# Kernel optimization log

Hardware: AMD Instinct MI355X
Metric: run time of the kernel (lower is better)

The kernel has to match this reference:

```python
import jax, jax.numpy as jnp
import numpy as np

B, SL = 16, 512
S = SL - 1            # context length after shift (length=1)
E = 256               # embedding_size / hidden_size
NH = 4                # num_heads
K = 4                 # conv1d_kernel_size
I = 2 * E             # mLSTM inner dim (_inner_embedding_dim = 2*E)
DHM = I // NH         # mLSTM head dim
DHS = E // NH         # sLSTM head dim
NB, BS = I // 4, 4    # qkv_proj_blocksize=4 block-diagonal projections
F = 384               # gated FFN up dim = round_up(1.3*256, 64)
NUM_SKILLS, NUM_Q = 500, 10000
EPS = 1e-5


def _ln(x, w):
    mu = x.mean(-1, keepdims=True)
    var = x.var(-1, keepdims=True)
    return (x - mu) / jnp.sqrt(var + EPS) * w


def _causal_dwconv(x, w, b):
    # x: (B,S,C), depthwise causal conv with kernel (C,K)
    xt = jnp.transpose(x, (0, 2, 1))
    y = jax.lax.conv_general_dilated(
        xt, w[:, None, :], (1,), [(K - 1, 0)],
        dimension_numbers=('NCH', 'OIH', 'NCH'),
        feature_group_count=x.shape[-1])
    return jnp.transpose(y, (0, 2, 1)) + b


def _headwise(x, w):
    # block-diagonal linear: w (NB, BS, BS)
    xb = x.reshape(x.shape[0], x.shape[1], NB, BS)
    return jnp.einsum('bsnd,nod->bsno', xb, w).reshape(x.shape)


def _forward(questions, responses, skills,
             q_embed, qa_embed, q_embed_diff, qa_embed_diff, difficult_param,
             ln0_w, m_up_w, m_up_b, m_conv_w, m_conv_b, m_q_w, m_k_w, m_v_w,
             m_ig_w, m_ig_b, m_fg_w, m_fg_b, m_outnorm_w, m_skip, m_down_w, m_down_b,
             ln1_w, s_conv_w, s_conv_b, s_gate_w, s_rec_w, s_bias, s_gn_w,
             ln2_w, ffn_up_w, ffn_up_b, ffn_down_w, ffn_down_b,
             postnorm_w, out_w1, out_b1, out_w2, out_b2, out_w3, out_b3):
    pid = questions[:, :-1]
    q_data = skills[:, :-1]
    q_shft = skills[:, 1:]
    target = (responses * (responses > -1).astype(responses.dtype))[:, :-1]

    q_e = q_embed[q_data]                              # (B,S,E)
    qa_e = qa_embed[target] + q_e
    pid_e = difficult_param[pid]                       # (B,S,1)
    q_e = q_e + pid_e * q_embed_diff[q_data]
    qa_e = qa_e + pid_e * qa_embed_diff[target]

    # ---- xLSTM stack: block 0 = mLSTM block, block 1 = sLSTM block + gated FFN ----
    x = qa_e  # dropout is identity in eval

    # mLSTM block: x = x + mlstm_layer(LN(x))
    h = _ln(x, ln0_w)
    up = h @ m_up_w.T + m_up_b                         # (B,S,2I)
    x_m, z = jnp.split(up, 2, axis=-1)
    xc = jax.nn.silu(_causal_dwconv(x_m, m_conv_w, m_conv_b))
    q = _headwise(xc, m_q_w)
    k = _headwise(xc, m_k_w)
    v = _headwise(x_m, m_v_w)
    ifin = jnp.concatenate([q, k, v], axis=-1)         # (B,S,3I)
    ig = jnp.einsum('bsf,hf->bhs', ifin, m_ig_w) + m_ig_b[None, :, None]
    fg = jnp.einsum('bsf,hf->bhs', ifin, m_fg_w) + m_fg_b[None, :, None]
    qh = q.reshape(B, S, NH, DHM).transpose(0, 2, 1, 3)
    kh = k.reshape(B, S, NH, DHM).transpose(0, 2, 1, 3)
    vh = v.reshape(B, S, NH, DHM).transpose(0, 2, 1, 3)
    # parallel stabilized mLSTM
    logf = jax.nn.log_sigmoid(fg)                      # (B,NH,S)
    cs = jnp.concatenate([jnp.zeros((B, NH, 1), logf.dtype), jnp.cumsum(logf, -1)], -1)
    dmat = cs[:, :, 1:, None] - cs[:, :, None, 1:]     # (B,NH,S,S): sum of logf over (s,t]
    ltr = jnp.tril(jnp.ones((S, S), bool))
    logD = jnp.where(ltr, dmat, -jnp.inf) + ig[:, :, None, :]
    maxD = jnp.max(logD, -1, keepdims=True)
    D = jnp.exp(logD - maxD)
    qk = jnp.einsum('bhtd,bhsd->bhts', qh, kh) * (DHM ** -0.5)
    C = qk * D
    norm = jnp.maximum(jnp.abs(C.sum(-1, keepdims=True)), jnp.exp(-maxD))
    hh = jnp.einsum('bhts,bhsd->bhtd', C / (norm + 1e-6), vh)
    # multi-head layernorm (per head over DHM), weight on flattened dim
    hn = (hh - hh.mean(-1, keepdims=True)) / jnp.sqrt(hh.var(-1, keepdims=True) + EPS)
    hflat = hn.transpose(0, 2, 1, 3).reshape(B, S, I) * m_outnorm_w
    hout = (hflat + m_skip * xc) * jax.nn.silu(z)
    x = x + (hout @ m_down_w.T + m_down_b)

    # sLSTM block: x = x + slstm_layer(LN(x)); x = x + ffn(LN(x))
    h = _ln(x, ln1_w)
    hc = jax.nn.silu(_causal_dwconv(h, s_conv_w, s_conv_b))
    hh4 = h.reshape(B, S, NH, DHS)
    hc4 = hc.reshape(B, S, NH, DHS)
    gi = jnp.einsum('bsnd,nod->bsno', hc4, s_gate_w[0])   # i,f from conv path
    gf = jnp.einsum('bsnd,nod->bsno', hc4, s_gate_w[1])
    gz = jnp.einsum('bsnd,nod->bsno', hh4, s_gate_w[2])   # z,o from x path
    go = jnp.einsum('bsnd,nod->bsno', hh4, s_gate_w[3])
    wx = jnp.stack([gi, gf, gz, go], axis=2) + s_bias[None, None]  # (B,S,4,NH,DHS)

    def step(carry, wx_t):
        y, c, n, m = carry
        raw = wx_t + jnp.einsum('bnd,gnde->bgne', y, s_rec_w)
        iraw, fraw, zraw, oraw = raw[:, 0], raw[:, 1], raw[:, 2], raw[:, 3]
        logfplusm = m + jax.nn.log_sigmoid(fraw)
        mnew = jnp.maximum(iraw, logfplusm)
        ig_ = jnp.exp(iraw - mnew)
        fg_ = jnp.exp(logfplusm - mnew)
        cnew = fg_ * c + ig_ * jnp.tanh(zraw)
        nnew = fg_ * n + ig_
        ynew = jax.nn.sigmoid(oraw) * cnew / nnew
        return (ynew, cnew, nnew, mnew), ynew

    z0 = jnp.zeros((B, NH, DHS), x.dtype)
    _, ys = jax.lax.scan(step, (z0, z0, z0, z0), jnp.swapaxes(wx, 0, 1))
    y = jnp.swapaxes(ys, 0, 1)                           # (B,S,NH,DHS)
    yn = (y - y.mean(-1, keepdims=True)) / jnp.sqrt(y.var(-1, keepdims=True) + EPS)
    x = x + yn.reshape(B, S, E) * s_gn_w

    # gated FFN (relu)
    h = _ln(x, ln2_w)
    gate, upf = jnp.split(h @ ffn_up_w.T + ffn_up_b, 2, axis=-1)
    x = x + (jax.nn.relu(gate) * upf) @ ffn_down_w.T + ffn_down_b

    d = _ln(x, postnorm_w)                               # post_blocks_norm

    fam = jnp.where((target == 1)[..., None], d, 0.0)
    unfam = jnp.where((target == 0)[..., None], d, 0.0)
    d2 = d - pid_e
    cq = jnp.concatenate([d2, q_e, fam, unfam], axis=-1)  # (B,S,4E)
    o = jax.nn.relu(cq @ out_w1.T + out_b1)
    o = jax.nn.relu(o @ out_w2.T + out_b2)
    probs = jax.nn.sigmoid(o @ out_w3.T + out_b3)
    pred = jnp.take_along_axis(probs, q_shft[..., None], axis=-1)[..., 0]
    return pred                                          # (B,S)


def setup_inputs():
    key = jax.random.key(0)
    ks = iter(jax.random.split(key, 64))
    def rn(shape, s=0.02):
        return jax.random.normal(next(ks), shape, jnp.float32) * s
    return dict(
        questions=jax.random.randint(next(ks), (B, SL), 0, NUM_Q),
        responses=jax.random.randint(next(ks), (B, SL), 0, 2),
        skills=jax.random.randint(next(ks), (B, SL), 0, NUM_SKILLS),
        attention_mask=jnp.ones((B, SL), jnp.int32),
        q_embed=rn((NUM_SKILLS, E), 1.0),
        qa_embed=rn((2, E), 1.0),
        q_embed_diff=rn((NUM_SKILLS + 1, E), 1.0),
        qa_embed_diff=rn((2 * NUM_SKILLS + 1, E), 1.0),
        difficult_param=rn((NUM_Q + 1, 1), 0.1),
        ln0_w=jnp.ones((E,)),
        m_up_w=rn((2 * I, E)), m_up_b=jnp.zeros((2 * I,)),
        m_conv_w=rn((I, K), 0.1), m_conv_b=jnp.zeros((I,)),
        m_q_w=rn((NB, BS, BS), 0.1), m_k_w=rn((NB, BS, BS), 0.1), m_v_w=rn((NB, BS, BS), 0.1),
        m_ig_w=rn((NH, 3 * I)), m_ig_b=jnp.zeros((NH,)),
        m_fg_w=rn((NH, 3 * I)), m_fg_b=jnp.zeros((NH,)),
        m_outnorm_w=jnp.ones((I,)), m_skip=jnp.ones((I,)),
        m_down_w=rn((E, I)), m_down_b=jnp.zeros((E,)),
        ln1_w=jnp.ones((E,)),
        s_conv_w=rn((E, K), 0.1), s_conv_b=jnp.zeros((E,)),
        s_gate_w=rn((4, NH, DHS, DHS), 0.1),
        s_rec_w=rn((4, NH, DHS, DHS), 0.05),
        s_bias=jnp.zeros((4, NH, DHS)),
        s_gn_w=jnp.ones((E,)),
        ln2_w=jnp.ones((E,)),
        ffn_up_w=rn((2 * F, E)), ffn_up_b=jnp.zeros((2 * F,)),
        ffn_down_w=rn((E, F)), ffn_down_b=jnp.zeros((E,)),
        postnorm_w=jnp.ones((E,)),
        out_w1=rn((2 * E, 4 * E)), out_b1=jnp.zeros((2 * E,)),
        out_w2=rn((E, 2 * E)), out_b2=jnp.zeros((E,)),
        out_w3=rn((NUM_SKILLS, E)), out_b3=jnp.zeros((NUM_SKILLS,)),
    )


def reference(questions, responses, skills, attention_mask,
              q_embed, qa_embed, q_embed_diff, qa_embed_diff, difficult_param,
              ln0_w, m_up_w, m_up_b, m_conv_w, m_conv_b, m_q_w, m_k_w, m_v_w,
              m_ig_w, m_ig_b, m_fg_w, m_fg_b, m_outnorm_w, m_skip, m_down_w, m_down_b,
              ln1_w, s_conv_w, s_conv_b, s_gate_w, s_rec_w, s_bias, s_gn_w,
              ln2_w, ffn_up_w, ffn_up_b, ffn_down_w, ffn_down_b,
              postnorm_w, out_w1, out_b1, out_w2, out_b2, out_w3, out_b3):
    return _forward(questions, responses, skills,
                    q_embed, qa_embed, q_embed_diff, qa_embed_diff, difficult_param,
                    ln0_w, m_up_w, m_up_b, m_conv_w, m_conv_b, m_q_w, m_k_w, m_v_w,
                    m_ig_w, m_ig_b, m_fg_w, m_fg_b, m_outnorm_w, m_skip, m_down_w, m_down_b,
                    ln1_w, s_conv_w, s_conv_b, s_gate_w, s_rec_w, s_bias, s_gn_w,
                    ln2_w, ffn_up_w, ffn_up_b, ffn_down_w, ffn_down_b,
                    postnorm_w, out_w1, out_b1, out_w2, out_b2, out_w3, out_b3)
```

## Files before the change

kernel.cpp:

```cpp
#include <hip/hip_runtime.h>
#include <hip/hip_bf16.h>

#define B_    16
#define SL_   512
#define S_    511
#define E_    256
#define NH_   4
#define I_    512
#define DHM_  128
#define DHS_  64
#define F_    384
#define NP_   8192
#define NROW  (B_*S_)
#define EPS_  1e-5f

typedef __hip_bfloat16 bf16;
typedef unsigned short u16;
typedef __bf16 bf16x8v __attribute__((ext_vector_type(8)));
typedef float  f32x4v  __attribute__((ext_vector_type(4)));

__device__ __forceinline__ float rcp_(float x){ return __builtin_amdgcn_rcpf(x); }
__device__ __forceinline__ float sig_(float x){ return rcp_(1.f+__expf(-x)); }
__device__ __forceinline__ float silu_(float x){ return x*sig_(x); }
__device__ __forceinline__ float logsig_(float x){ return fminf(x,0.f) - __logf(1.f + __expf(-fabsf(x))); }
__device__ __forceinline__ float expneg_(float x){ return __expf(fminf(x,0.f)); }
__device__ __forceinline__ float expclamp_(float x){ return __expf(fminf(fmaxf(x,-80.f),80.f)); }
__device__ __forceinline__ float tanh_(float x){ return 1.f - 2.f*rcp_(__expf(2.f*x)+1.f); }

__device__ __forceinline__ void cvt_split8(const float* __restrict__ p, bf16x8v& hv, bf16x8v& lv){
  float4 u = *(const float4*)p;
  float4 w = *(const float4*)(p+4);
  float x[8] = {u.x,u.y,u.z,u.w,w.x,w.y,w.z,w.w};
  union { bf16x8v v; u16 s[8]; } H, L;
  #pragma unroll
  for(int j=0;j<8;j++){
    bf16 hh = __float2bfloat16(x[j]);
    float hf = __bfloat162float(hh);
    bf16 ll = __float2bfloat16(x[j]-hf);
    __builtin_memcpy(&H.s[j],&hh,2);
    __builtin_memcpy(&L.s[j],&ll,2);
  }
  hv=H.v; lv=L.v;
}

__global__ __launch_bounds__(256) void k_cvt16(const float* __restrict__ src, bf16* __restrict__ dst, int n){
  int i=blockIdx.x*256+threadIdx.x;
  if(i<n) dst[i]=__float2bfloat16(src[i]);
}
__global__ __launch_bounds__(256) void k_cvt16i(const float* __restrict__ src, bf16* __restrict__ dst){
  int i=blockIdx.x*256+threadIdx.x;
  int rp=i>>8, c=i&255;
  int j=rp>>1, p=rp&1;
  dst[i]=__float2bfloat16(src[(size_t)(j + p*F_)*E_ + c]);
}
__global__ __launch_bounds__(256) void k_cvtsplit(const float* __restrict__ src,
  bf16* __restrict__ hi, bf16* __restrict__ lo, int n){
  int i=blockIdx.x*256+threadIdx.x;
  if(i<n){
    float v=src[i];
    bf16 h=__float2bfloat16(v);
    hi[i]=h;
    lo[i]=__float2bfloat16(v-__bfloat162float(h));
  }
}
__global__ __launch_bounds__(256) void k_wtrans(const float* __restrict__ src, float* __restrict__ dst){
  int i = blockIdx.x*256+threadIdx.x;
  int blk = i>>12;
  int d = (i>>6)&63;
  int e = i&63;
  dst[(size_t)(blk*64+d)*64+e] = src[(size_t)(blk*64+e)*64+d];
}

__global__ __launch_bounds__(256) void k_wfrag(const float* __restrict__ rw, bf16* __restrict__ wf){
  int i = blockIdx.x*256+threadIdx.x;
  int j  = i&7;
  int l  = (i>>3)&63;
  int kf = (i>>9)&1;
  int t  = (i>>10)&15;
  int n  = i>>14;
  int g = t>>2;
  int e = (t&3)*16 + (l&15);
  int d = (l>>4)*16 + kf*8 + j;
  wf[i] = __float2bfloat16(rw[((size_t)((g*4+n)*64 + d))*64 + e]);
}

__global__ __launch_bounds__(256) void k_embed(
  const int* __restrict__ questions, const int* __restrict__ responses, const int* __restrict__ skills,
  const float* __restrict__ q_embed, const float* __restrict__ qa_embed,
  const float* __restrict__ q_embed_diff, const float* __restrict__ qa_embed_diff,
  const float* __restrict__ difficult_param, const float* __restrict__ ln0w,
  float* __restrict__ x, float* __restrict__ qe,
  bf16* __restrict__ h_hi, bf16* __restrict__ h_lo,
  float* __restrict__ pide, int* __restrict__ tgt, int* __restrict__ qsh)
{
  __shared__ float red[256];
  int r = blockIdx.x; int e = threadIdx.x;
  float xa = 0.f;
  if (r < NROW){
    int b = r / S_, s = r % S_;
    int pid  = questions[b*SL_+s];
    int qd   = skills[b*SL_+s];
    int resp = responses[b*SL_+s];
    int t    = (resp > -1) ? resp : 0;
    float pe = difficult_param[pid];
    float q0 = q_embed[qd*E_+e];
    xa = q0 + qa_embed[t*E_+e] + pe*qa_embed_diff[t*E_+e];
    float qn = q0 + pe*q_embed_diff[qd*E_+e];
    x[(size_t)r*E_+e]=xa; qe[(size_t)r*E_+e]=qn;
    if (e==0){ pide[r]=pe; tgt[r]=t; qsh[r]=skills[b*SL_+s+1]; }
  } else {
    x[(size_t)r*E_+e]=0.f; qe[(size_t)r*E_+e]=0.f;
    if (e==0){ pide[r]=0.f; tgt[r]=-7; qsh[r]=0; }
  }
  red[e]=xa; __syncthreads();
  for(int s2=128;s2>0;s2>>=1){ if(e<s2) red[e]+=red[e+s2]; __syncthreads(); }
  float mu = red[0]*(1.f/E_); __syncthreads();
  float d = xa-mu;
  red[e]=d*d; __syncthreads();
  for(int s2=128;s2>0;s2>>=1){ if(e<s2) red[e]+=red[e+s2]; __syncthreads(); }
  float var = red[0]*(1.f/E_);
  float o = d*rsqrtf(var+EPS_)*ln0w[e];
  bf16 hv = __float2bfloat16(o);
  h_hi[(size_t)r*E_+e] = hv;
  h_lo[(size_t)r*E_+e] = __float2bfloat16(o-__bfloat162float(hv));
}

__global__ __launch_bounds__(256) void k_ln(
  const float* __restrict__ in, const float* __restrict__ w, float* __restrict__ out)
{
  __shared__ float red[256];
  int r = blockIdx.x, t = threadIdx.x;
  float v = in[(size_t)r*E_+t];
  red[t]=v; __syncthreads();
  for(int s=128;s>0;s>>=1){ if(t<s) red[t]+=red[t+s]; __syncthreads(); }
  float mu = red[0]*(1.f/E_); __syncthreads();
  float d = v-mu;
  red[t]=d*d; __syncthreads();
  for(int s=128;s>0;s>>=1){ if(t<s) red[t]+=red[t+s]; __syncthreads(); }
  float var = red[0]*(1.f/E_);
  out[(size_t)r*E_+t] = d*rsqrtf(var+EPS_)*w[t];
}

__global__ __launch_bounds__(256) void k_gemm16s(
  const bf16* __restrict__ Ah, const bf16* __restrict__ Al,
  const bf16* __restrict__ Bh, const bf16* __restrict__ Bl,
  const float* __restrict__ bias, float* __restrict__ C, int M, int K)
{
  int tid=threadIdx.x;
  int wave=tid>>6, lane=tid&63;
  int wr=wave>>1, wc=wave&1;
  int row0=blockIdx.y*64 + wr*32;
  int col0=blockIdx.x*64 + wc*32;
  int lrow = lane&15, lq = lane>>4;
  f32x4v acc[2][2] = {};
  size_t aoff = (size_t)(row0+lrow)*K + lq*8;
  size_t boff = (size_t)(col0+lrow)*K + lq*8;
  for(int k0=0;k0<K;k0+=32){
    bf16x8v ah0=*(const bf16x8v*)(Ah+aoff+k0), ah1=*(const bf16x8v*)(Ah+aoff+(size_t)16*K+k0);
    bf16x8v al0=*(const bf16x8v*)(Al+aoff+k0), al1=*(const bf16x8v*)(Al+aoff+(size_t)16*K+k0);
    bf16x8v bh0=*(const bf16x8v*)(Bh+boff+k0), bh1=*(const bf16x8v*)(Bh+boff+(size_t)16*K+k0);
    bf16x8v bl0=*(const bf16x8v*)(Bl+boff+k0), bl1=*(const bf16x8v*)(Bl+boff+(size_t)16*K+k0);
    acc[0][0]=__builtin_amdgcn_mfma_f32_16x16x32_bf16(ah0,bh0,acc[0][0],0,0,0);
    acc[0][1]=__builtin_amdgcn_mfma_f32_16x16x32_bf16(ah0,bh1,acc[0][1],0,0,0);
    acc[1][0]=__builtin_amdgcn_mfma_f32_16x16x32_bf16(ah1,bh0,acc[1][0],0,0,0);
    acc[1][1]=__builtin_amdgcn_mfma_f32_16x16x32_bf16(ah1,bh1,acc[1][1],0,0,0);
    acc[0][0]=__builtin_amdgcn_mfma_f32_16x16x32_bf16(ah0,bl0,acc[0][0],0,0,0);
    acc[0][1]=__builtin_amdgcn_mfma_f32_16x16x32_bf16(ah0,bl1,acc[0][1],0,0,0);
    acc[1][0]=__builtin_amdgcn_mfma_f32_16x16x32_bf16(ah1,bl0,acc[1][0],0,0,0);
    acc[1][1]=__builtin_amdgcn_mfma_f32_16x16x32_bf16(ah1,bl1,acc[1][1],0,0,0);
    acc[0][0]=__builtin_amdgcn_mfma_f32_16x16x32_bf16(al0,bh0,acc[0][0],0,0,0);
    acc[0][1]=__builtin_amdgcn_mfma_f32_16x16x32_bf16(al0,bh1,acc[0][1],0,0,0);
    acc[1][0]=__builtin_amdgcn_mfma_f32_16x16x32_bf16(al1,bh0,acc[1][0],0,0,0);
    acc[1][1]=__builtin_amdgcn_mfma_f32_16x16x32_bf16(al1,bh1,acc[1][1],0,0,0);
  }
  #pragma unroll
  for(int mi=0;mi<2;mi++){
    #pragma unroll
    for(int ni=0;ni<2;ni++){
      #pragma unroll
      for(int r=0;r<4;r++){
        int row=row0+mi*16+lq*4+r;
        int col=col0+ni*16+lrow;
        C[(size_t)row*M+col]=acc[mi][ni][r] + bias[col];
      }
    }
  }
}

__global__ __launch_bounds__(256) void k_gemm16(
  const bf16* __restrict__ A, const bf16* __restrict__ Bw,
  const float* __restrict__ bias, const float* __restrict__ resid,
  float* __restrict__ C, bf16* __restrict__ C16,
  int M, int K, int relu)
{
  int tid=threadIdx.x;
  int wave=tid>>6, lane=tid&63;
  int wr=wave>>1, wc=wave&1;
  int row0=blockIdx.y*64 + wr*32;
  int col0=blockIdx.x*64 + wc*32;
  int lrow = lane&15, lq = lane>>4;
  f32x4v acc[2][2] = {};
  const bf16* Abase = A  + (size_t)(row0+lrow)*K + lq*8;
  const bf16* Bbase = Bw + (size_t)(col0+lrow)*K + lq*8;
  for(int k0=0;k0<K;k0+=32){
    bf16x8v a0 = *(const bf16x8v*)(Abase + k0);
    bf16x8v a1 = *(const bf16x8v*)(Abase + (size_t)16*K + k0);
    bf16x8v b0 = *(const bf16x8v*)(Bbase + k0);
    bf16x8v b1 = *(const bf16x8v*)(Bbase + (size_t)16*K + k0);
    acc[0][0]=__builtin_amdgcn_mfma_f32_16x16x32_bf16(a0,b0,acc[0][0],0,0,0);
    acc[0][1]=__builtin_amdgcn_mfma_f32_16x16x32_bf16(a0,b1,acc[0][1],0,0,0);
    acc[1][0]=__builtin_amdgcn_mfma_f32_16x16x32_bf16(a1,b0,acc[1][0],0,0,0);
    acc[1][1]=__builtin_amdgcn_mfma_f32_16x16x32_bf16(a1,b1,acc[1][1],0,0,0);
  }
  #pragma unroll
  for(int mi=0;mi<2;mi++){
    #pragma unroll
    for(int ni=0;ni<2;ni++){
      #pragma unroll
      for(int r=0;r<4;r++){
        int row=row0+mi*16+lq*4+r;
        int col=col0+ni*16+lrow;
        float v=acc[mi][ni][r] + (bias? bias[col]:0.f);
        if(relu) v=fmaxf(v,0.f);
        if(resid) v += resid[(size_t)row*M+col];
        if(C)   C[(size_t)row*M+col]=v;
        if(C16) C16[(size_t)row*M+col]=__float2bfloat16(v);
      }
    }
  }
}

__global__ __launch_bounds__(256) void k_gemm16f(
  const bf16* __restrict__ A, const bf16* __restrict__ Bw,
  const float* __restrict__ bias, bf16* __restrict__ out, int K)
{
  int tid=threadIdx.x;
  int wave=tid>>6, lane=tid&63;
  int wr=wave>>1, wc=wave&1;
  int row0=blockIdx.y*64 + wr*32;
  int col0=blockIdx.x*64 + wc*32;
  int lrow = lane&15, lq = lane>>4;
  f32x4v acc[2][2] = {};
  const bf16* Abase = A  + (size_t)(row0+lrow)*K + lq*8;
  const bf16* Bbase = Bw + (size_t)(col0+lrow)*K + lq*8;
  for(int k0=0;k0<K;k0+=32){
    bf16x8v a0 = *(const bf16x8v*)(Abase + k0);
    bf16x8v a1 = *(const bf16x8v*)(Abase + (size_t)16*K + k0);
    bf16x8v b0 = *(const bf16x8v*)(Bbase + k0);
    bf16x8v b1 = *(const bf16x8v*)(Bbase + (size_t)16*K + k0);
    acc[0][0]=__builtin_amdgcn_mfma_f32_16x16x32_bf16(a0,b0,acc[0][0],0,0,0);
    acc[0][1]=__builtin_amdgcn_mfma_f32_16x16x32_bf16(a0,b1,acc[0][1],0,0,0);
    acc[1][0]=__builtin_amdgcn_mfma_f32_16x16x32_bf16(a1,b0,acc[1][0],0,0,0);
    acc[1][1]=__builtin_amdgcn_mfma_f32_16x16x32_bf16(a1,b1,acc[1][1],0,0,0);
  }
  #pragma unroll
  for(int mi=0;mi<2;mi++){
    #pragma unroll
    for(int ni=0;ni<2;ni++){
      #pragma unroll
      for(int r=0;r<4;r++){
        int row=row0+mi*16+lq*4+r;
        int col=col0+ni*16+lrow;
        float v=acc[mi][ni][r] + bias[(col>>1) + (col&1)*F_];
        float o = __shfl_xor(v, 1, 64);
        if(!(lrow&1)){
          out[(size_t)row*F_ + (col>>1)] = __float2bfloat16(fmaxf(v,0.f)*o);
        }
      }
    }
  }
}

__global__ __launch_bounds__(256) void k_conv_silu(
  const float* __restrict__ in, int ild, const float* __restrict__ w, const float* __restrict__ bws,
  float* __restrict__ out, int old_, int C)
{
  int i = blockIdx.x*256 + threadIdx.x;
  int r = i / C, c = i % C;
  if (r >= NP_) return;
  float acc = 0.f;
  if (r < NROW) {
    int b=r/S_, s=r%S_;
    acc = bws[c];
    #pragma unroll
    for(int j=0;j<4;j++){
      int ss=s-3+j;
      if(ss>=0) acc += w[c*4+j] * in[(size_t)(b*S_+ss)*ild + c];
    }
    acc = silu_(acc);
  }
  out[(size_t)r*old_ + c] = acc;
}

__global__ __launch_bounds__(256) void k_headwise(
  const float* __restrict__ xc, const float* __restrict__ xm, int xmld,
  const float* __restrict__ wq, const float* __restrict__ wk, const float* __restrict__ wv,
  float* __restrict__ q, float* __restrict__ k, float* __restrict__ v)
{
  int i=blockIdx.x*256+threadIdx.x;
  int r=i/I_, c=i%I_;
  if(r>=NP_) return;
  size_t oi=(size_t)r*I_+c;
  if(r>=NROW){ q[oi]=0.f; k[oi]=0.f; v[oi]=0.f; return; }
  int n=c>>2, o=c&3;
  const float* xcr = xc + (size_t)r*I_ + n*4;
  const float* xmr = xm + (size_t)r*xmld + n*4;
  float aq=0.f, ak=0.f, av=0.f;
  #pragma unroll
  for(int d=0;d<4;d++){
    float xcv=xcr[d], xmv=xmr[d];
    aq += xcv*wq[(n*4+o)*4+d];
    ak += xcv*wk[(n*4+o)*4+d];
    av += xmv*wv[(n*4+o)*4+d];
  }
  q[oi]=aq; k[oi]=ak; v[oi]=av;
}

__global__ __launch_bounds__(256) void k_igfg(
  const float* __restrict__ q, const float* __restrict__ k, const float* __restrict__ v,
  const float* __restrict__ wig, const float* __restrict__ big,
  const float* __restrict__ wfg, const float* __restrict__ bfg,
  float* __restrict__ igb, float* __restrict__ fgb)
{
  int r=blockIdx.x;
  int wid=threadIdx.x>>6, lane=threadIdx.x&63;
  int b=r/S_, s=r%S_;
  for(int c=wid; c<8; c+=4){
    int h=c>>1; int isfg=c&1;
    const float* w = isfg? wfg : wig;
    float acc=0.f;
    for(int f=lane; f<1536; f+=64){
      float val = (f<512)? q[(size_t)r*512+f]
                : (f<1024)? k[(size_t)r*512+f-512]
                : v[(size_t)r*512+f-1024];
      acc += val*w[h*1536+f];
    }
    for(int m=32;m;m>>=1) acc+=__shfl_xor(acc,m,64);
    if(lane==0){
      if(isfg) fgb[(b*4+h)*512+s]=acc+bfg[h];
      else     igb[(b*4+h)*512+s]=acc+big[h];
    }
  }
}

__global__ __launch_bounds__(256) void k_decay(
  const float* __restrict__ igb, const float* __restrict__ fgb,
  float* __restrict__ cs1, float* __restrict__ g, float* __restrict__ M)
{
  int bh = blockIdx.x; int tid = threadIdx.x;
  __shared__ float buf[512];
  __shared__ float buf2[512];
  for (int s=tid; s<512; s+=256)
    buf[s] = (s<S_) ? logsig_(fgb[bh*512+s]) : 0.f;
  __syncthreads();
  for (int off=1; off<512; off<<=1){
    int s0=tid, s1=tid+256;
    float v0 = buf[s0] + ((s0>=off)? buf[s0-off] : 0.f);
    float v1 = buf[s1] + ((s1>=off)? buf[s1-off] : 0.f);
    __syncthreads();
    buf[s0]=v0; buf[s1]=v1;
    __syncthreads();
  }
  for (int s=tid; s<512; s+=256){
    float c = buf[s];
    if (s<S_){
      cs1[bh*512+s]=c;
      float gv = igb[bh*512+s]-c;
      g[bh*512+s]=gv;
      buf2[s]=gv;
    } else buf2[s] = -3.4e38f;
  }
  __syncthreads();
  for (int off=1; off<512; off<<=1){
    int s0=tid, s1=tid+256;
    float v0 = fmaxf(buf2[s0], (s0>=off)? buf2[s0-off] : -3.4e38f);
    float v1 = fmaxf(buf2[s1], (s1>=off)? buf2[s1-off] : -3.4e38f);
    __syncthreads();
    buf2[s0]=v0; buf2[s1]=v1;
    __syncthreads();
  }
  for (int s=tid; s<S_; s+=256) M[bh*512+s] = buf2[s];
}

#define TQ 32
#define TS 32
__global__ __launch_bounds__(256) void k_attn(
  const float* __restrict__ q, const float* __restrict__ k, const float* __restrict__ v,
  const float* __restrict__ cs1, const float* __restrict__ g, const float* __restrict__ M,
  const float* __restrict__ onw, float* __restrict__ hflat)
{
  __shared__ __align__(16) u16 vThi[128][40];
  __shared__ __align__(16) u16 vTlo[128][40];
  __shared__ __align__(16) u16 phi[32][40];
  __shared__ __align__(16) u16 plo[32][40];
  __shared__ float MtS[32], cssS[32], normS[32], muS[32], rsS[32];
  __shared__ float lsumW[2][32], sumA[2][32], sumB[2][32];

  int tq = blockIdx.x, bh = blockIdx.y;
  int b = bh>>2, h = bh&3;
  int tid = threadIdx.x;
  int wv = tid>>6;
  int tw = wv&1, sw = wv>>1;
  int l = tid&63;
  int lr = l&15, lg = l>>4;
  int t0 = tq*TQ;
  const float sc = 0.08838834764831843f;

  if (tid < 32){
    int t = t0 + tid; int tc = (t<S_)? t : (S_-1);
    MtS[tid]  = M[bh*512 + tc];
    cssS[tid] = cs1[bh*512 + tc];
  }

  bf16x8v qh[4], ql[4];
  {
    const float* qrow = q + ((size_t)(b*S_ + t0 + tw*16 + lr))*512 + h*128 + lg*8;
    #pragma unroll
    for(int k0=0;k0<4;k0++) cvt_split8(qrow + (size_t)k0*32, qh[k0], ql[k0]);
  }

  f32x4v accpv[4] = {};
  float lsum[4] = {0.f,0.f,0.f,0.f};

  int t1 = min(t0+TQ, S_);
  int sp = tid>>4, dl = tid&15;

  __syncthreads();

  for (int s0=0; s0<t1; s0+=TS){
    bf16x8v kh[4], kl2[4];
    {
      const float* krow = k + ((size_t)(b*S_ + s0 + sw*16 + lr))*512 + h*128 + lg*8;
      #pragma unroll
      for(int k0=0;k0<4;k0++) cvt_split8(krow + (size_t)k0*32, kh[k0], kl2[k0]);
    }
    float va[8], vb[8];
    {
      const float* vap = v + ((size_t)(b*S_ + s0 + 2*sp))*512 + h*128 + dl;
      const float* vbp = vap + 512;
      #pragma unroll
      for(int j=0;j<8;j++){ va[j]=vap[16*j]; vb[j]=vbp[16*j]; }
    }
    float g_s = g[bh*512 + s0 + sw*16 + lr];

    f32x4v cqk = {0.f,0.f,0.f,0.f};
    #pragma unroll
    for(int k0=0;k0<4;k0++){
      cqk = __builtin_amdgcn_mfma_f32_16x16x32_bf16(qh[k0], kh[k0],  cqk, 0,0,0);
      cqk = __builtin_amdgcn_mfma_f32_16x16x32_bf16(qh[k0], kl2[k0], cqk, 0,0,0);
      cqk = __builtin_amdgcn_mfma_f32_16x16x32_bf16(ql[k0], kh[k0],  cqk, 0,0,0);
    }

    int s_g = s0 + sw*16 + lr;
    u16 pw_h[4], pw_l[4];
    #pragma unroll
    for(int r=0;r<4;r++){
      int tl = tw*16 + lg*4 + r;
      int t_row = t0 + tl;
      float wvv = ((s_g <= t_row) && (t_row < S_)) ? cqk[r]*sc*expneg_(g_s - MtS[tl]) : 0.f;
      lsum[r] += wvv;
      bf16 hh = __float2bfloat16(wvv);
      float hf = __bfloat162float(hh);
      bf16 ll = __float2bfloat16(wvv - hf);
      __builtin_memcpy(&pw_h[r], &hh, 2);
      __builtin_memcpy(&pw_l[r], &ll, 2);
    }

    __syncthreads();

    #pragma unroll
    for(int r=0;r<4;r++){
      int tl = tw*16 + lg*4 + r;
      phi[tl][sw*16 + lr] = pw_h[r];
      plo[tl][sw*16 + lr] = pw_l[r];
    }
    {
      unsigned* vh32 = (unsigned*)&vThi[0][0];
      unsigned* vl32 = (unsigned*)&vTlo[0][0];
      #pragma unroll
      for(int j=0;j<8;j++){
        int d = dl + 16*j;
        bf16 ha=__float2bfloat16(va[j]);
        bf16 hb=__float2bfloat16(vb[j]);
        float haf=__bfloat162float(ha), hbf=__bfloat162float(hb);
        bf16 la=__float2bfloat16(va[j]-haf);
        bf16 lb=__float2bfloat16(vb[j]-hbf);
        u16 hau,hbu,lau,lbu;
        __builtin_memcpy(&hau,&ha,2); __builtin_memcpy(&hbu,&hb,2);
        __builtin_memcpy(&lau,&la,2); __builtin_memcpy(&lbu,&lb,2);
        vh32[d*20 + sp] = (unsigned)hau | ((unsigned)hbu<<16);
        vl32[d*20 + sp] = (unsigned)lau | ((unsigned)lbu<<16);
      }
    }

    __syncthreads();

    bf16x8v pah = *(const bf16x8v*)((const void*)(&phi[tw*16 + lr][0] + lg*8));
    bf16x8v pal = *(const bf16x8v*)((const void*)(&plo[tw*16 + lr][0] + lg*8));
    #pragma unroll
    for(int fd=0; fd<4; fd++){
      bf16x8v vbh = *(const bf16x8v*)((const void*)(&vThi[sw*64 + fd*16 + lr][0] + lg*8));
      bf16x8v vbl = *(const bf16x8v*)((const void*)(&vTlo[sw*64 + fd*16 + lr][0] + lg*8));
      accpv[fd] = __builtin_amdgcn_mfma_f32_16x16x32_bf16(pah, vbh, accpv[fd], 0,0,0);
      accpv[fd] = __builtin_amdgcn_mfma_f32_16x16x32_bf16(pah, vbl, accpv[fd], 0,0,0);
      accpv[fd] = __builtin_amdgcn_mfma_f32_16x16x32_bf16(pal, vbh, accpv[fd], 0,0,0);
    }
  }

  #pragma unroll
  for(int r=0;r<4;r++){
    #pragma unroll
    for(int m=1;m<16;m<<=1) lsum[r] += __shfl_xor(lsum[r], m, 16);
  }
  if (lr==0){
    #pragma unroll
    for(int r=0;r<4;r++) lsumW[sw][tw*16 + lg*4 + r] = lsum[r];
  }
  __syncthreads();
  if (tid < 32){
    float ls = lsumW[0][tid] + lsumW[1][tid];
    float maxD = cssS[tid] + MtS[tid];
    float nrm = fmaxf(fabsf(ls), expclamp_(-maxD));
    normS[tid] = rcp_(nrm + 1e-6f);
  }
  __syncthreads();

  float o_[4][4];
  float srow[4]={0.f,0.f,0.f,0.f}, sq[4]={0.f,0.f,0.f,0.f};
  #pragma unroll
  for(int r=0;r<4;r++){
    float scl = normS[tw*16 + lg*4 + r];
    #pragma unroll
    for(int fd=0;fd<4;fd++){
      float o = accpv[fd][r]*scl;
      o_[fd][r] = o;
      srow[r] += o; sq[r] += o*o;
    }
  }
  #pragma unroll
  for(int r=0;r<4;r++){
    #pragma unroll
    for(int m=1;m<16;m<<=1){ srow[r]+=__shfl_xor(srow[r],m,16); sq[r]+=__shfl_xor(sq[r],m,16); }
  }
  if (lr==0){
    #pragma unroll
    for(int r=0;r<4;r++){ sumA[sw][tw*16+lg*4+r]=srow[r]; sumB[sw][tw*16+lg*4+r]=sq[r]; }
  }
  __syncthreads();
  if (tid < 32){
    float mu = (sumA[0][tid]+sumA[1][tid])*(1.f/128.f);
    float ex2= (sumB[0][tid]+sumB[1][tid])*(1.f/128.f);
    muS[tid]=mu;
    rsS[tid]=rsqrtf(fmaxf(ex2 - mu*mu, 0.f)+EPS_);
  }
  __syncthreads();

  #pragma unroll
  for(int fd=0; fd<4; fd++){
    int d = sw*64 + fd*16 + lr;
    float ow = onw[h*128 + d];
    #pragma unroll
    for(int r=0;r<4;r++){
      int tl = tw*16 + lg*4 + r;
      int t = t0 + tl;
      if (t < S_)
        hflat[((size_t)(b*S_+t))*1024 + h*128 + d] = (o_[fd][r]-muS[tl])*rsS[tl]*ow;
    }
  }
}

__global__ __launch_bounds__(256) void k_hout(
  const float* __restrict__ A, const float* __restrict__ xc, const float* __restrict__ skip,
  bf16* __restrict__ out16)
{
  int i=blockIdx.x*256+threadIdx.x;
  int r=i/512, c=i%512;
  float hf=A[(size_t)r*1024+c];
  float z =A[(size_t)r*1024+512+c];
  out16[(size_t)r*512+c] = __float2bfloat16((hf + skip[c]*xc[(size_t)r*512+c]) * silu_(z));
}

#define WXR 64
__global__ __launch_bounds__(256,2) void k_wx(
  const float* __restrict__ h, const float* __restrict__ hc,
  const float* __restrict__ gwT, const float* __restrict__ gb,
  float* __restrict__ wx)
{
  int rt = blockIdx.x, g = blockIdx.y;
  int tid = threadIdx.x;
  int n = tid>>6, e = tid&63;
  const float* src = (g<2)? hc : h;
  __shared__ __align__(16) float hs[WXR][260];
  float W[64];
  #pragma unroll
  for(int d=0;d<64;d++) W[d] = gwT[(size_t)(((g*4+n)*64+d))*64 + e];
  float bias = gb[(g*4+n)*64+e];
  int row0 = rt*WXR;
  for(int idx=tid; idx<WXR*64; idx+=256){
    int rr = idx>>6, cc4 = (idx&63)*4;
    *(float4*)&hs[rr][cc4] = *(const float4*)(src + (size_t)(row0+rr)*256 + cc4);
  }
  __syncthreads();
  #pragma unroll 4
  for(int rr=0; rr<WXR; ++rr){
    int r = row0+rr;
    if (r>=NROW) break;
    const float* hrow = &hs[rr][n*64];
    float a0=0,a1=0,a2=0,a3=0;
    #pragma unroll
    for(int d=0;d<64;d+=4){
      float4 hv = *(const float4*)&hrow[d];
      a0+=hv.x*W[d]; a1+=hv.y*W[d+1]; a2+=hv.z*W[d+2]; a3+=hv.w*W[d+3];
    }
    int b=r/S_, s=r%S_;
    wx[(((size_t)(b*4+n)*512 + s)*256) + e*4 + g] = bias + ((a0+a1)+(a2+a3));
  }
}

__global__ __launch_bounds__(256,1) void k_scan(
  const float* __restrict__ wx, const bf16* __restrict__ wf, float* __restrict__ y_out)
{
  int bn = blockIdx.x; int b = bn>>2, n = bn&3;
  int tid = threadIdx.x;
  int w = tid>>6;
  int l = tid&63;
  int q = l>>4;
  int el = l&15;
  int e  = w*16 + el;

  __shared__ __align__(16) unsigned short ybuf[2][64];

  if (tid < 128) ((unsigned short*)ybuf)[tid] = 0;
  __syncthreads();

  bf16x8v Wf2[4][2];
  #pragma unroll
  for(int g=0; g<4; ++g){
    #pragma unroll
    for(int kf=0; kf<2; ++kf){
      Wf2[g][kf] = *(const bf16x8v*)(wf + ((size_t)((n*16 + (4*g+w))*2 + kf)*64 + l)*8);
    }
  }

  const float* wxBase = wx + ((size_t)bn*512)*256 + e*4;
  float* yst = y_out + (size_t)(b*S_)*256 + n*64 + e;

  float4 p0,p1,p2,p3;
  p0 = *(const float4*)(wxBase + (size_t)0*256);
  p1 = *(const float4*)(wxBase + (size_t)1*256);
  p2 = *(const float4*)(wxBase + (size_t)2*256);
  p3 = *(const float4*)(wxBase + (size_t)3*256);

  f32x4v z4 = {0.f,0.f,0.f,0.f};
  float c=0.f, nn=0.f, pm=1.f;

  for (int s=0; s<S_; ++s){
    int p = s&1;
    bf16x8v a0 = *(const bf16x8v*)&ybuf[p][16*q];
    bf16x8v a1 = *(const bf16x8v*)&ybuf[p][16*q+8];

    f32x4v acc0,acc1,acc2,acc3;
    acc0 = __builtin_amdgcn_mfma_f32_16x16x32_bf16(a0, Wf2[0][0], z4, 0,0,0);
    acc1 = __builtin_amdgcn_mfma_f32_16x16x32_bf16(a0, Wf2[1][0], z4, 0,0,0);
    acc2 = __builtin_amdgcn_mfma_f32_16x16x32_bf16(a0, Wf2[2][0], z4, 0,0,0);
    acc3 = __builtin_amdgcn_mfma_f32_16x16x32_bf16(a0, Wf2[3][0], z4, 0,0,0);
    acc0 = __builtin_amdgcn_mfma_f32_16x16x32_bf16(a1, Wf2[0][1], acc0, 0,0,0);
    acc1 = __builtin_amdgcn_mfma_f32_16x16x32_bf16(a1, Wf2[1][1], acc1, 0,0,0);
    acc2 = __builtin_amdgcn_mfma_f32_16x16x32_bf16(a1, Wf2[2][1], acc2, 0,0,0);
    acc3 = __builtin_amdgcn_mfma_f32_16x16x32_bf16(a1, Wf2[3][1], acc3, 0,0,0);

    float4 wg = p0; p0=p1; p1=p2; p2=p3;
    { int sp = s+4; if (sp>510) sp=510;
      p3 = *(const float4*)(wxBase + (size_t)sp*256); }

    float iraw=acc0[0]+wg.x, fraw=acc1[0]+wg.y, zraw=acc2[0]+wg.z, oraw=acc3[0]+wg.w;

    float pe  = __expf(fminf(iraw, 80.f));
    float ef  = __expf(-fraw);
    float e2z = __expf(2.f*zraw);
    float eo  = __expf(-oraw);
    float sf  = rcp_(1.f+ef);
    float ps  = pm*sf;
    float pn  = fmaxf(fmaxf(pe, ps), 1e-30f);
    float rpn = rcp_(pn);
    float fg  = ps*rpn;
    float ig  = pe*rpn;
    float th  = 1.f - 2.f*rcp_(e2z+1.f);
    c  = fg*c + ig*th;
    nn = fmaxf(fg*nn + ig, 1e-30f);
    float y = rcp_(1.f+eo) * c * rcp_(nn);
    pm = pn;

    bf16 hb = __float2bfloat16(y);
    unsigned short hbits; __builtin_memcpy(&hbits,&hb,2);
    if (l < 16){
      ybuf[p^1][e] = hbits;
      yst[(size_t)s*256] = y;
    }
    asm volatile("s_waitcnt lgkmcnt(0)" ::: "memory");
    __builtin_amdgcn_s_barrier();
    asm volatile("" ::: "memory");
    __builtin_amdgcn_sched_barrier(0);
  }
}

__global__ __launch_bounds__(256) void k_ynadd_ln2(
  const float* __restrict__ y, const float* __restrict__ gn,
  float* __restrict__ x, const float* __restrict__ ln2w, bf16* __restrict__ h16)
{
  __shared__ float red[256];
  int r=blockIdx.x, t=threadIdx.x;
  float xv = x[(size_t)r*256+t];
  if (r < NROW){
    float v=y[(size_t)r*256+t];
    float s=v;
    for(int m=32;m;m>>=1) s+=__shfl_xor(s,m,64);
    float mu=s*(1.f/64.f);
    float d=v-mu;
    float q=d*d;
    for(int m=32;m;m>>=1) q+=__shfl_xor(q,m,64);
    float var=q*(1.f/64.f);
    xv += d*rsqrtf(var+EPS_)*gn[t];
    x[(size_t)r*256+t]=xv;
  }
  red[t]=xv; __syncthreads();
  for(int s=128;s>0;s>>=1){ if(t<s) red[t]+=red[t+s]; __syncthreads(); }
  float mu2=red[0]*(1.f/E_); __syncthreads();
  float dd=xv-mu2;
  red[t]=dd*dd; __syncthreads();
  for(int s=128;s>0;s>>=1){ if(t<s) red[t]+=red[t+s]; __syncthreads(); }
  float var2=red[0]*(1.f/E_);
  h16[(size_t)r*256+t]=__float2bfloat16(dd*rsqrtf(var2+EPS_)*ln2w[t]);
}

__global__ __launch_bounds__(256) void k_cq_ln(
  const float* __restrict__ x, const float* __restrict__ pw,
  const float* __restrict__ qe, const float* __restrict__ pide, const int* __restrict__ tgt,
  bf16* __restrict__ cq)
{
  __shared__ float red[256];
  int r=blockIdx.x, t=threadIdx.x;
  float v = x[(size_t)r*256+t];
  red[t]=v; __syncthreads();
  for(int s=128;s>0;s>>=1){ if(t<s) red[t]+=red[t+s]; __syncthreads(); }
  float mu=red[0]*(1.f/E_); __syncthreads();
  float d=v-mu;
  red[t]=d*d; __syncthreads();
  for(int s=128;s>0;s>>=1){ if(t<s) red[t]+=red[t+s]; __syncthreads(); }
  float var=red[0]*(1.f/E_);
  float dv = d*rsqrtf(var+EPS_)*pw[t];
  float pe=pide[r]; int tg=tgt[r];
  size_t base=(size_t)r*1024;
  cq[base+t]=__float2bfloat16(dv-pe);
  cq[base+256+t]=__float2bfloat16(qe[(size_t)r*256+t]);
  cq[base+512+t]=__float2bfloat16((tg==1)? dv:0.f);
  cq[base+768+t]=__float2bfloat16((tg==0)? dv:0.f);
}

__global__ __launch_bounds__(256) void k_final(
  const float* __restrict__ o2, const float* __restrict__ w3, const float* __restrict__ b3,
  const int* __restrict__ qsh, float* __restrict__ out)
{
  __shared__ float red[256];
  int r=blockIdx.x, t=threadIdx.x;
  int qi=qsh[r];
  float p=o2[(size_t)r*256+t]*w3[(size_t)qi*256+t];
  red[t]=p; __syncthreads();
  for(int s=128;s>0;s>>=1){ if(t<s) red[t]+=red[t+s]; __syncthreads(); }
  if(t==0) out[r]=sig_(red[0]+b3[qi]);
}

extern "C" void kernel_launch(void* const* d_in, const int* in_sizes, int n_in,
                              void* d_out, int out_size, void* d_ws, size_t ws_size,
                              hipStream_t stream) {
  const int* questions = (const int*)d_in[0];
  const int* responses = (const int*)d_in[1];
  const int* skills    = (const int*)d_in[2];
  const float* q_embed       = (const float*)d_in[4];
  const float* qa_embed      = (const float*)d_in[5];
  const float* q_embed_diff  = (const float*)d_in[6];
  const float* qa_embed_diff = (const float*)d_in[7];
  const float* difficult_param=(const float*)d_in[8];
  const float* ln0_w   = (const float*)d_in[9];
  const float* m_up_w  = (const float*)d_in[10];
  const float* m_up_b  = (const float*)d_in[11];
  const float* m_conv_w= (const float*)d_in[12];
  const float* m_conv_b= (const float*)d_in[13];
  const float* m_q_w   = (const float*)d_in[14];
  const float* m_k_w   = (const float*)d_in[15];
  const float* m_v_w   = (const float*)d_in[16];
  const float* m_ig_w  = (const float*)d_in[17];
  const float* m_ig_b  = (const float*)d_in[18];
  const float* m_fg_w  = (const float*)d_in[19];
  const float* m_fg_b  = (const float*)d_in[20];
  const float* m_outnorm_w=(const float*)d_in[21];
  const float* m_skip  = (const float*)d_in[22];
  const float* m_down_w= (const float*)d_in[23];
  const float* m_down_b= (const float*)d_in[24];
  const float* ln1_w   = (const float*)d_in[25];
  const float* s_conv_w= (const float*)d_in[26];
  const float* s_conv_b= (const float*)d_in[27];
  const float* s_gate_w= (const float*)d_in[28];
  const float* s_rec_w = (const float*)d_in[29];
  const float* s_bias  = (const float*)d_in[30];
  const float* s_gn_w  = (const float*)d_in[31];
  const float* ln2_w   = (const float*)d_in[32];
  const float* ffn_up_w= (const float*)d_in[33];
  const float* ffn_up_b= (const float*)d_in[34];
  const float* ffn_down_w=(const float*)d_in[35];
  const float* ffn_down_b=(const float*)d_in[36];
  const float* postnorm_w=(const float*)d_in[37];
  const float* out_w1  = (const float*)d_in[38];
  const float* out_b1  = (const float*)d_in[39];
  const float* out_w2  = (const float*)d_in[40];
  const float* out_b2  = (const float*)d_in[41];
  const float* out_w3  = (const float*)d_in[42];
  const float* out_b3  = (const float*)d_in[43];

  float* ws = (float*)d_ws;
  const size_t R = (size_t)NP_*256;
  float* x    = ws;
  float* qe   = ws + R;
  float* h    = ws + 2*R;
  float* t256 = ws + 3*R;
  float* A    = ws + 4*R;
  float* Bb   = ws + 8*R;
  float* Cb   = ws + 10*R;
  float* Db   = ws + 12*R;
  float* Eb   = ws + 14*R;
  float* pide = ws + 16*R;
  int*   tgt  = (int*)(ws + 16*R + NP_);
  int*   qsh  = (int*)(ws + 16*R + 2*NP_);
  float* igb  = ws + 16*R + 3*NP_;
  float* fgb  = igb + 64*512;
  float* cs1  = fgb + 64*512;
  float* gdec = cs1 + 64*512;
  float* Mrun = gdec + 64*512;
  bf16* wpool = (bf16*)(Mrun + 64*512);
  bf16* m_down_w16  = wpool;
  bf16* ffn_up_w16  = m_down_w16 + 256*512;
  bf16* ffn_down_w16= ffn_up_w16 + 768*256;
  bf16* out_w1_16   = ffn_down_w16 + 256*384;
  bf16* out_w2_16   = out_w1_16 + 512*1024;
  bf16* h16         = out_w2_16 + 256*512;
  bf16* m_up_whi    = h16 + (size_t)NP_*256;
  bf16* m_up_wlo    = m_up_whi + 1024*256;
  float* gwT        = (float*)(m_up_wlo + 1024*256);
  bf16* wfrag       = (bf16*)(gwT + 16*64*64);
  bf16* hout16 = (bf16*)Db;
  bf16* ffg16  = (bf16*)Db;
  bf16* cq16   = (bf16*)Eb;
  bf16* b16    = (bf16*)Cb;
  bf16* h_hi   = (bf16*)t256;
  bf16* h_lo   = h_hi + (size_t)NP_*256;

  k_cvt16<<<(256*512+255)/256,256,0,stream>>>(m_down_w,  m_down_w16,  256*512);
  k_cvt16i<<<(768*256)/256,256,0,stream>>>(ffn_up_w, ffn_up_w16);
  k_cvt16<<<(256*384+255)/256,256,0,stream>>>(ffn_down_w,ffn_down_w16,256*384);
  k_cvt16<<<(512*1024+255)/256,256,0,stream>>>(out_w1,   out_w1_16,   512*1024);
  k_cvt16<<<(256*512+255)/256,256,0,stream>>>(out_w2,    out_w2_16,   256*512);
  k_cvtsplit<<<(1024*256+255)/256,256,0,stream>>>(m_up_w, m_up_whi, m_up_wlo, 1024*256);
  k_wtrans<<<(16*64*64)/256,256,0,stream>>>(s_gate_w, gwT);
  k_wfrag<<<65536/256,256,0,stream>>>(s_rec_w, wfrag);

  k_embed<<<NP_,256,0,stream>>>(questions,responses,skills,q_embed,qa_embed,
      q_embed_diff,qa_embed_diff,difficult_param, ln0_w, x,qe, h_hi,h_lo, pide,tgt,qsh);
  k_gemm16s<<<dim3(1024/64,NP_/64),256,0,stream>>>(h_hi,h_lo, m_up_whi,m_up_wlo, m_up_b, A, 1024,256);
  k_conv_silu<<<(NP_*512)/256,256,0,stream>>>(A,1024, m_conv_w,m_conv_b, Bb,512,512);
  k_headwise<<<(NP_*512)/256,256,0,stream>>>(Bb, A,1024, m_q_w,m_k_w,m_v_w, Cb,Db,Eb);
  k_igfg<<<NROW,256,0,stream>>>(Cb,Db,Eb, m_ig_w,m_ig_b,m_fg_w,m_fg_b, igb,fgb);
  k_decay<<<64,256,0,stream>>>(igb,fgb, cs1,gdec,Mrun);
  k_attn<<<dim3((S_+TQ-1)/TQ, B_*NH_),256,0,stream>>>(Cb,Db,Eb, cs1,gdec,Mrun, m_outnorm_w, A);
  k_hout<<<(NP_*512)/256,256,0,stream>>>(A, Bb, m_skip, hout16);
  k_gemm16<<<dim3(256/64,NP_/64),256,0,stream>>>(hout16, m_down_w16, m_down_b, x, x, (bf16*)nullptr, 256,512,0);
  k_ln<<<NP_,256,0,stream>>>(x, ln1_w, h);
  k_conv_silu<<<(NP_*256)/256,256,0,stream>>>(h,256, s_conv_w,s_conv_b, Bb,256,256);
  k_wx<<<dim3(128,4),256,0,stream>>>(h, Bb, gwT, s_bias, A);
  k_scan<<<64,256,0,stream>>>(A, wfrag, Cb);
  k_ynadd_ln2<<<NP_,256,0,stream>>>(Cb, s_gn_w, x, ln2_w, h16);
  k_gemm16f<<<dim3(768/64,NP_/64),256,0,stream>>>(h16, ffn_up_w16, ffn_up_b, ffg16, 256);
  k_gemm16<<<dim3(256/64,NP_/64),256,0,stream>>>(ffg16, ffn_down_w16, ffn_down_b, x, x, (bf16*)nullptr, 256,384,0);
  k_cq_ln<<<NP_,256,0,stream>>>(x, postnorm_w, qe, pide, tgt, cq16);
  k_gemm16<<<dim3(512/64,NP_/64),256,0,stream>>>(cq16, out_w1_16, out_b1, (const float*)nullptr, (float*)nullptr, b16, 512,1024,1);
  k_gemm16<<<dim3(256/64,NP_/64),256,0,stream>>>(b16, out_w2_16, out_b2, (const float*)nullptr, t256, (bf16*)nullptr, 256,512,1);
  k_final<<<NROW,256,0,stream>>>(t256, out_w3, out_b3, qsh, (float*)d_out);
}
```

Measured before the change: 867.3 us.

## Pre-split q/k/v into bf16 hi/lo in headwise and fuse output gating into attention

The headwise projection now writes q, k and v directly as bf16 hi/lo pairs, so the attention kernel loads ready MFMA operands and no longer converts fp32 tiles again on every key block. The k_hout kernel is removed and its skip-add and SiLU gating are folded into the attention epilogue, which writes bf16 output directly. A memset zeroes the padding rows of that output. This avoids repeated conversions in attention and an extra pass over an fp32 intermediate, at the cost of separate hi/lo buffers and scattered stores in the epilogue. The hout16 buffer now aliases the h buffer.

```diff
diff --git a/kernel.cpp b/kernel.cpp
--- a/kernel.cpp
+++ b/kernel.cpp
@@ -26,22 +26,6 @@
 __device__ __forceinline__ float expneg_(float x){ return __expf(fminf(x,0.f)); }
 __device__ __forceinline__ float expclamp_(float x){ return __expf(fminf(fmaxf(x,-80.f),80.f)); }
 __device__ __forceinline__ float tanh_(float x){ return 1.f - 2.f*rcp_(__expf(2.f*x)+1.f); }
-
-__device__ __forceinline__ void cvt_split8(const float* __restrict__ p, bf16x8v& hv, bf16x8v& lv){
-  float4 u = *(const float4*)p;
-  float4 w = *(const float4*)(p+4);
-  float x[8] = {u.x,u.y,u.z,u.w,w.x,w.y,w.z,w.w};
-  union { bf16x8v v; u16 s[8]; } H, L;
-  #pragma unroll
-  for(int j=0;j<8;j++){
-    bf16 hh = __float2bfloat16(x[j]);
-    float hf = __bfloat162float(hh);
-    bf16 ll = __float2bfloat16(x[j]-hf);
-    __builtin_memcpy(&H.s[j],&hh,2);
-    __builtin_memcpy(&L.s[j],&ll,2);
-  }
-  hv=H.v; lv=L.v;
-}
 
 __global__ __launch_bounds__(256) void k_cvt16(const float* __restrict__ src, bf16* __restrict__ dst, int n){
   int i=blockIdx.x*256+threadIdx.x;
@@ -295,13 +279,19 @@
 __global__ __launch_bounds__(256) void k_headwise(
   const float* __restrict__ xc, const float* __restrict__ xm, int xmld,
   const float* __restrict__ wq, const float* __restrict__ wk, const float* __restrict__ wv,
-  float* __restrict__ q, float* __restrict__ k, float* __restrict__ v)
+  bf16* __restrict__ qhi, bf16* __restrict__ qlo,
+  bf16* __restrict__ khi, bf16* __restrict__ klo,
+  bf16* __restrict__ vhi, bf16* __restrict__ vlo)
 {
   int i=blockIdx.x*256+threadIdx.x;
   int r=i/I_, c=i%I_;
   if(r>=NP_) return;
   size_t oi=(size_t)r*I_+c;
-  if(r>=NROW){ q[oi]=0.f; k[oi]=0.f; v[oi]=0.f; return; }
+  if(r>=NROW){
+    bf16 z=__float2bfloat16(0.f);
+    qhi[oi]=z; qlo[oi]=z; khi[oi]=z; klo[oi]=z; vhi[oi]=z; vlo[oi]=z;
+    return;
+  }
   int n=c>>2, o=c&3;
   const float* xcr = xc + (size_t)r*I_ + n*4;
   const float* xmr = xm + (size_t)r*xmld + n*4;
@@ -313,11 +303,15 @@
     ak += xcv*wk[(n*4+o)*4+d];
     av += xmv*wv[(n*4+o)*4+d];
   }
-  q[oi]=aq; k[oi]=ak; v[oi]=av;
+  bf16 qh=__float2bfloat16(aq); qhi[oi]=qh; qlo[oi]=__float2bfloat16(aq-__bfloat162float(qh));
+  bf16 kh=__float2bfloat16(ak); khi[oi]=kh; klo[oi]=__float2bfloat16(ak-__bfloat162float(kh));
+  bf16 vh=__float2bfloat16(av); vhi[oi]=vh; vlo[oi]=__float2bfloat16(av-__bfloat162float(vh));
 }
 
 __global__ __launch_bounds__(256) void k_igfg(
-  const float* __restrict__ q, const float* __restrict__ k, const float* __restrict__ v,
+  const bf16* __restrict__ qhi, const bf16* __restrict__ qlo,
+  const bf16* __restrict__ khi, const bf16* __restrict__ klo,
+  const bf16* __restrict__ vhi, const bf16* __restrict__ vlo,
   const float* __restrict__ wig, const float* __restrict__ big,
   const float* __restrict__ wfg, const float* __restrict__ bfg,
   float* __restrict__ igb, float* __restrict__ fgb)
@@ -330,9 +324,10 @@
     const float* w = isfg? wfg : wig;
     float acc=0.f;
     for(int f=lane; f<1536; f+=64){
-      float val = (f<512)? q[(size_t)r*512+f]
-                : (f<1024)? k[(size_t)r*512+f-512]
-                : v[(size_t)r*512+f-1024];
+      float val;
+      if (f<512)       val = __bfloat162float(qhi[(size_t)r*512+f])      + __bfloat162float(qlo[(size_t)r*512+f]);
+      else if (f<1024) val = __bfloat162float(khi[(size_t)r*512+f-512])  + __bfloat162float(klo[(size_t)r*512+f-512]);
+      else             val = __bfloat162float(vhi[(size_t)r*512+f-1024]) + __bfloat162float(vlo[(size_t)r*512+f-1024]);
       acc += val*w[h*1536+f];
     }
     for(int m=32;m;m>>=1) acc+=__shfl_xor(acc,m,64);
@@ -385,9 +380,13 @@
 #define TQ 32
 #define TS 32
 __global__ __launch_bounds__(256) void k_attn(
-  const float* __restrict__ q, const float* __restrict__ k, const float* __restrict__ v,
+  const bf16* __restrict__ qhi, const bf16* __restrict__ qlo,
+  const bf16* __restrict__ khi, const bf16* __restrict__ klo,
+  const bf16* __restrict__ vhi, const bf16* __restrict__ vlo,
   const float* __restrict__ cs1, const float* __restrict__ g, const float* __restrict__ M,
-  const float* __restrict__ onw, float* __restrict__ hflat)
+  const float* __restrict__ onw, const float* __restrict__ skip,
+  const float* __restrict__ xc, const float* __restrict__ zA,
+  bf16* __restrict__ out16)
 {
   __shared__ __align__(16) u16 vThi[128][40];
   __shared__ __align__(16) u16 vTlo[128][40];
@@ -414,9 +413,12 @@
 
   bf16x8v qh[4], ql[4];
   {
-    const float* qrow = q + ((size_t)(b*S_ + t0 + tw*16 + lr))*512 + h*128 + lg*8;
-    #pragma unroll
-    for(int k0=0;k0<4;k0++) cvt_split8(qrow + (size_t)k0*32, qh[k0], ql[k0]);
+    size_t qoff = ((size_t)(b*S_ + t0 + tw*16 + lr))*512 + h*128 + lg*8;
+    #pragma unroll
+    for(int k0=0;k0<4;k0++){
+      qh[k0] = *(const bf16x8v*)(qhi + qoff + k0*32);
+      ql[k0] = *(const bf16x8v*)(qlo + qoff + k0*32);
+    }
   }
 
   f32x4v accpv[4] = {};
@@ -430,16 +432,22 @@
   for (int s0=0; s0<t1; s0+=TS){
     bf16x8v kh[4], kl2[4];
     {
-      const float* krow = k + ((size_t)(b*S_ + s0 + sw*16 + lr))*512 + h*128 + lg*8;
+      size_t koff = ((size_t)(b*S_ + s0 + sw*16 + lr))*512 + h*128 + lg*8;
       #pragma unroll
-      for(int k0=0;k0<4;k0++) cvt_split8(krow + (size_t)k0*32, kh[k0], kl2[k0]);
-    }
-    float va[8], vb[8];
+      for(int k0=0;k0<4;k0++){
+        kh[k0]  = *(const bf16x8v*)(khi + koff + k0*32);
+        kl2[k0] = *(const bf16x8v*)(klo + koff + k0*32);
+      }
+    }
+    u16 vha[8], vhb[8], vla[8], vlb[8];
     {
-      const float* vap = v + ((size_t)(b*S_ + s0 + 2*sp))*512 + h*128 + dl;
-      const float* vbp = vap + 512;
+      const u16* ha = (const u16*)vhi + ((size_t)(b*S_ + s0 + 2*sp))*512 + h*128 + dl;
+      const u16* la = (const u16*)vlo + ((size_t)(b*S_ + s0 + 2*sp))*512 + h*128 + dl;
       #pragma unroll
-      for(int j=0;j<8;j++){ va[j]=vap[16*j]; vb[j]=vbp[16*j]; }
+      for(int j=0;j<8;j++){
+        vha[j]=ha[16*j]; vhb[j]=ha[512+16*j];
+        vla[j]=la[16*j]; vlb[j]=la[512+16*j];
+      }
     }
     float g_s = g[bh*512 + s0 + sw*16 + lr];
 
@@ -480,16 +488,8 @@
       #pragma unroll
       for(int j=0;j<8;j++){
         int d = dl + 16*j;
-        bf16 ha=__float2bfloat16(va[j]);
-        bf16 hb=__float2bfloat16(vb[j]);
-        float haf=__bfloat162float(ha), hbf=__bfloat162float(hb);
-        bf16 la=__float2bfloat16(va[j]-haf);
-        bf16 lb=__float2bfloat16(vb[j]-hbf);
-        u16 hau,hbu,lau,lbu;
-        __builtin_memcpy(&hau,&ha,2); __builtin_memcpy(&hbu,&hb,2);
-        __builtin_memcpy(&lau,&la,2); __builtin_memcpy(&lbu,&lb,2);
-        vh32[d*20 + sp] = (unsigned)hau | ((unsigned)hbu<<16);
-        vl32[d*20 + sp] = (unsigned)lau | ((unsigned)lbu<<16);
+        vh32[d*20 + sp] = (unsigned)vha[j] | ((unsigned)vhb[j]<<16);
+        vl32[d*20 + sp] = (unsigned)vla[j] | ((unsigned)vlb[j]<<16);
       }
     }
 
@@ -559,25 +559,20 @@
   for(int fd=0; fd<4; fd++){
     int d = sw*64 + fd*16 + lr;
     float ow = onw[h*128 + d];
+    float sk = skip[h*128 + d];
     #pragma unroll
     for(int r=0;r<4;r++){
       int tl = tw*16 + lg*4 + r;
       int t = t0 + tl;
-      if (t < S_)
-        hflat[((size_t)(b*S_+t))*1024 + h*128 + d] = (o_[fd][r]-muS[tl])*rsS[tl]*ow;
-    }
-  }
-}
-
-__global__ __launch_bounds__(256) void k_hout(
-  const float* __restrict__ A, const float* __restrict__ xc, const float* __restrict__ skip,
-  bf16* __restrict__ out16)
-{
-  int i=blockIdx.x*256+threadIdx.x;
-  int r=i/512, c=i%512;
-  float hf=A[(size_t)r*1024+c];
-  float z =A[(size_t)r*1024+512+c];
-  out16[(size_t)r*512+c] = __float2bfloat16((hf + skip[c]*xc[(size_t)r*512+c]) * silu_(z));
+      if (t < S_){
+        size_t row = (size_t)(b*S_+t);
+        float hf = (o_[fd][r]-muS[tl])*rsS[tl]*ow;
+        float xcv = xc[row*512 + h*128 + d];
+        float zv  = zA[row*1024 + 512 + h*128 + d];
+        out16[row*512 + h*128 + d] = __float2bfloat16((hf + sk*xcv)*silu_(zv));
+      }
+    }
+  }
 }
 
 #define WXR 64
@@ -847,7 +842,10 @@
   bf16* m_up_wlo    = m_up_whi + 1024*256;
   float* gwT        = (float*)(m_up_wlo + 1024*256);
   bf16* wfrag       = (bf16*)(gwT + 16*64*64);
-  bf16* hout16 = (bf16*)Db;
+  bf16* q_hi = (bf16*)Cb;  bf16* q_lo = q_hi + (size_t)NP_*512;
+  bf16* k_hi = (bf16*)Db;  bf16* k_lo = k_hi + (size_t)NP_*512;
+  bf16* v_hi = (bf16*)Eb;  bf16* v_lo = v_hi + (size_t)NP_*512;
+  bf16* hout16 = (bf16*)h;
   bf16* ffg16  = (bf16*)Db;
   bf16* cq16   = (bf16*)Eb;
   bf16* b16    = (bf16*)Cb;
@@ -867,11 +865,13 @@
       q_embed_diff,qa_embed_diff,difficult_param, ln0_w, x,qe, h_hi,h_lo, pide,tgt,qsh);
   k_gemm16s<<<dim3(1024/64,NP_/64),256,0,stream>>>(h_hi,h_lo, m_up_whi,m_up_wlo, m_up_b, A, 1024,256);
   k_conv_silu<<<(NP_*512)/256,256,0,stream>>>(A,1024, m_conv_w,m_conv_b, Bb,512,512);
-  k_headwise<<<(NP_*512)/256,256,0,stream>>>(Bb, A,1024, m_q_w,m_k_w,m_v_w, Cb,Db,Eb);
-  k_igfg<<<NROW,256,0,stream>>>(Cb,Db,Eb, m_ig_w,m_ig_b,m_fg_w,m_fg_b, igb,fgb);
+  k_headwise<<<(NP_*512)/256,256,0,stream>>>(Bb, A,1024, m_q_w,m_k_w,m_v_w,
+      q_hi,q_lo, k_hi,k_lo, v_hi,v_lo);
+  k_igfg<<<NROW,256,0,stream>>>(q_hi,q_lo, k_hi,k_lo, v_hi,v_lo, m_ig_w,m_ig_b,m_fg_w,m_fg_b, igb,fgb);
   k_decay<<<64,256,0,stream>>>(igb,fgb, cs1,gdec,Mrun);
-  k_attn<<<dim3((S_+TQ-1)/TQ, B_*NH_),256,0,stream>>>(Cb,Db,Eb, cs1,gdec,Mrun, m_outnorm_w, A);
-  k_hout<<<(NP_*512)/256,256,0,stream>>>(A, Bb, m_skip, hout16);
+  hipMemsetAsync(hout16 + (size_t)NROW*512, 0, (size_t)(NP_-NROW)*512*sizeof(bf16), stream);
+  k_attn<<<dim3((S_+TQ-1)/TQ, B_*NH_),256,0,stream>>>(q_hi,q_lo, k_hi,k_lo, v_hi,v_lo,
+      cs1,gdec,Mrun, m_outnorm_w, m_skip, Bb, A, hout16);
   k_gemm16<<<dim3(256/64,NP_/64),256,0,stream>>>(hout16, m_down_w16, m_down_b, x, x, (bf16*)nullptr, 256,512,0);
   k_ln<<<NP_,256,0,stream>>>(x, ln1_w, h);
   k_conv_silu<<<(NP_*256)/256,256,0,stream>>>(h,256, s_conv_w,s_conv_b, Bb,256,256);
```

Result: no change. 869.6 us (+0.3%).
